# Optimization experiments

Measured on AMD Instinct MI355X. Metric: run time of the kernel, lower is better.

Reference implementation:

```python
import jax, jax.numpy as jnp
import numpy as np

NORM_EPS = 1e-6
QUANT_EPS = 1e-8


def setup_inputs() -> dict:
    key = jax.random.key(0)
    k1, k2 = jax.random.split(key)
    B, S, D_IN, D_OUT = 2, 4096, 2048, 2048
    x = jax.random.normal(k1, (B, S, D_IN), dtype=jnp.float32)
    # master fp32 weights (kaiming-uniform-ish scale)
    weight = jax.random.uniform(k2, (D_OUT, D_IN), dtype=jnp.float32,
                                minval=-1.0, maxval=1.0) * (1.0 / np.sqrt(D_IN))
    norm_weight = jnp.ones((D_IN,), dtype=jnp.float32)
    return {"x": x, "weight": weight, "norm_weight": norm_weight}


def _rmsnorm(x, gain):
    rms = jnp.sqrt(jnp.mean(x * x, axis=-1, keepdims=True) + NORM_EPS)
    return x / rms * gain


def _ternary_quantize(w):
    gamma = jnp.mean(jnp.abs(w))                       # absmean scale (scalar)
    w_q = jnp.clip(jnp.round(w / (gamma + QUANT_EPS)), -1.0, 1.0)
    return w_q, gamma


def reference(x, weight, norm_weight):
    # 1) RMSNorm input
    xn = _rmsnorm(x, norm_weight)
    # 2) ternary-quantize weights {-1,0,+1} with absmean gamma
    w_q, gamma = _ternary_quantize(weight)
    # 3) matmul with ternary weights, 4) scale by gamma
    # xn: [B,S,Din], w_q: [Dout,Din] -> [B,S,Dout]
    return jnp.einsum('bsd,od->bso', xn, w_q) * gamma
```

## Files before the change

### kernel.cpp

```cpp
#include <hip/hip_runtime.h>
#include <hip/hip_bf16.h>
#include <stdint.h>

typedef unsigned short u16;
typedef signed char i8;

#define D_INNER 2048
#define D_OUTER 2048
#define MROWS   8192
#define W_ELEMS (D_OUTER * D_INNER)
#define NPART   1024

#define BM 256
#define BN 256
#define BK 128
#define NKT (D_INNER / BK)
#define SLOT_BYTES 65536
#define LDS_TOTAL  131072

typedef __attribute__((ext_vector_type(4))) float f32x4;
typedef __attribute__((ext_vector_type(4))) int   i32x4;
typedef __attribute__((ext_vector_type(16))) int  i32x16;

__global__ __launch_bounds__(256) void prep_kernel(const float* __restrict__ x,
                            const float* __restrict__ g,
                            const float* __restrict__ w,
                            i8* __restrict__ xn, float* __restrict__ srow,
                            float* __restrict__ partials) {
  int t = threadIdx.x;
  int lane = t & 63, wvi = t >> 6;

  if (blockIdx.x >= MROWS / 4) {
    __shared__ float red[4];
    int p = blockIdx.x - MROWS / 4;
    int base = p * 1024;
    float s = 0.f;
#pragma unroll
    for (int r = 0; r < 4; ++r) {
      f32x4 v = ((const f32x4*)w)[base + r * 256 + t];
      s += fabsf(v[0]) + fabsf(v[1]) + fabsf(v[2]) + fabsf(v[3]);
    }
    for (int off = 32; off; off >>= 1) s += __shfl_down(s, off, 64);
    if (lane == 0) red[wvi] = s;
    __syncthreads();
    if (t == 0) partials[p] = red[0] + red[1] + red[2] + red[3];
    return;
  }

  int row = blockIdx.x * 4 + wvi;
  const f32x4* xr = (const f32x4*)(x + (size_t)row * D_INNER);
  const f32x4* gr = (const f32x4*)g;
  i8* xo = xn + (size_t)row * D_INNER;

  f32x4 v[8], gv[8];
#pragma unroll
  for (int r = 0; r < 8; ++r) {
    v[r]  = __builtin_nontemporal_load(&xr[lane + r * 64]);
    gv[r] = gr[lane + r * 64];
  }
  float s = 0.f, m = 0.f;
#pragma unroll
  for (int r = 0; r < 8; ++r) {
    s += v[r][0]*v[r][0] + v[r][1]*v[r][1] + v[r][2]*v[r][2] + v[r][3]*v[r][3];
    m = fmaxf(m, fmaxf(fmaxf(fabsf(v[r][0]*gv[r][0]), fabsf(v[r][1]*gv[r][1])),
                       fmaxf(fabsf(v[r][2]*gv[r][2]), fabsf(v[r][3]*gv[r][3]))));
  }
#pragma unroll
  for (int off = 32; off; off >>= 1) {
    s += __shfl_xor(s, off, 64);
    m = fmaxf(m, __shfl_xor(m, off, 64));
  }
  float invr = 1.0f / sqrtf(s * (1.0f / (float)D_INNER) + 1e-6f);
  float amax = fmaxf(m * invr, 1e-12f);
  float step = amax * (1.0f / 127.0f);
  float qs   = 127.0f / amax;
  if (lane == 0) srow[row] = step;

#pragma unroll
  for (int r = 0; r < 8; ++r) {
    char4 q;
    float qv;
    qv = fminf(127.f, fmaxf(-127.f, rintf(v[r][0]*invr*gv[r][0]*qs))); q.x = (i8)(int)qv;
    qv = fminf(127.f, fmaxf(-127.f, rintf(v[r][1]*invr*gv[r][1]*qs))); q.y = (i8)(int)qv;
    qv = fminf(127.f, fmaxf(-127.f, rintf(v[r][2]*invr*gv[r][2]*qs))); q.z = (i8)(int)qv;
    qv = fminf(127.f, fmaxf(-127.f, rintf(v[r][3]*invr*gv[r][3]*qs))); q.w = (i8)(int)qv;
    ((char4*)xo)[lane + r * 64] = q;
  }
}

__global__ __launch_bounds__(256) void quant_kernel(const float* __restrict__ w,
                             const float* __restrict__ partials,
                             float* __restrict__ gamma_out, i8* __restrict__ wq) {
  f32x4 pv = ((const f32x4*)partials)[threadIdx.x];
  double d = (double)pv[0] + (double)pv[1] + (double)pv[2] + (double)pv[3];
  for (int off = 32; off; off >>= 1) d += __shfl_down(d, off, 64);
  __shared__ double red[4];
  int lane = threadIdx.x & 63, wvi = threadIdx.x >> 6;
  if (lane == 0) red[wvi] = d;
  __syncthreads();
  double total = red[0] + red[1] + red[2] + red[3];
  float gamma = (float)(total * (1.0 / (double)W_ELEMS));
  float inv = 1.0f / (gamma + 1e-8f);
  if (blockIdx.x == 0 && threadIdx.x == 0) *gamma_out = gamma;

  int tid = blockIdx.x * blockDim.x + threadIdx.x;
  int stride = gridDim.x * blockDim.x;
  for (int i = tid; i < W_ELEMS / 4; i += stride) {
    f32x4 v = ((const f32x4*)w)[i];
    char4 q;
    q.x = (i8)(int)fminf(1.f, fmaxf(-1.f, rintf(v[0] * inv)));
    q.y = (i8)(int)fminf(1.f, fmaxf(-1.f, rintf(v[1] * inv)));
    q.z = (i8)(int)fminf(1.f, fmaxf(-1.f, rintf(v[2] * inv)));
    q.w = (i8)(int)fminf(1.f, fmaxf(-1.f, rintf(v[3] * inv)));
    ((char4*)wq)[i] = q;
  }
}

#define GLDS(SRC, DST) __builtin_amdgcn_global_load_lds( \
    (const __attribute__((address_space(1))) void*)(SRC), \
    (__attribute__((address_space(3))) void*)(DST), 16, 0, 0)
#define WAITVM(N) asm volatile("s_waitcnt vmcnt(" #N ")")
#define BAR()     __builtin_amdgcn_s_barrier()
#define FENCE()   __builtin_amdgcn_sched_barrier(0)

__global__ __launch_bounds__(256, 1) void gemm_bt(const i8* __restrict__ A,
                                                  const i8* __restrict__ Bw,
                                                  const float* __restrict__ gamma_p,
                                                  const float* __restrict__ srow,
                                                  float* __restrict__ C) {
  extern __shared__ i8 lds[];

  int f   = blockIdx.y * 8 + blockIdx.x;
  int xcd = f & 7;
  int gg  = f >> 3;
  int orig = xcd * 32 + gg;
  int nb  = orig & 7;
  int mb  = orig >> 3;
  int bm0 = mb * BM;
  int bn0 = nb * BN;

  int tid  = threadIdx.x;
  int lane = tid & 63;
  int wv   = tid >> 6;
  int wr   = wv >> 1;
  int wc   = wv & 1;
  int l31  = lane & 31;
  int hi   = lane >> 5;

  const i8* Ag = A  + (size_t)bm0 * D_INNER;
  const i8* Bg = Bw + (size_t)bn0 * D_INNER;

  size_t srcx = (size_t)(tid >> 3) * D_INNER + (((tid & 7) ^ ((tid >> 3) & 7)) << 4);

  int rdA = (wr * 128 + l31) * BK;
  int rdB = 32768 + (wc * 128 + l31) * BK;
  int swz[4];
#pragma unroll
  for (int ks = 0; ks < 4; ++ks)
    swz[ks] = (((ks << 1) | hi) ^ (l31 & 7)) << 4;

  i32x16 acc[4][4] = {};
  i32x4 bf_[4][4];

#define GLDS_A(T_, RR, S_) \
    GLDS(Ag + srcx + (size_t)(RR) * (32 * D_INNER) + (size_t)(T_) * BK, \
         lds + (S_) * SLOT_BYTES + (RR) * 4096 + tid * 16)
#define GLDS_B(T_, RR, S_) \
    GLDS(Bg + srcx + (size_t)(RR) * (32 * D_INNER) + (size_t)(T_) * BK, \
         lds + (S_) * SLOT_BYTES + 32768 + (RR) * 4096 + tid * 16)

#define PHASE(T_, P_, DS_) do { \
    if (DS_) { \
      if ((P_) == 0) { GLDS_A(T_+1, 0, (T_+1)&1); GLDS_A(T_+1, 1, (T_+1)&1); \
                       GLDS_A(T_+1, 2, (T_+1)&1); GLDS_B(T_+1, 0, (T_+1)&1); \
                       GLDS_B(T_+1, 1, (T_+1)&1); GLDS_B(T_+1, 2, (T_+1)&1); } \
      if ((P_) == 1) { GLDS_A(T_+1, 3, (T_+1)&1); GLDS_A(T_+1, 4, (T_+1)&1); \
                       GLDS_A(T_+1, 5, (T_+1)&1); GLDS_B(T_+1, 3, (T_+1)&1); \
                       GLDS_B(T_+1, 4, (T_+1)&1); GLDS_B(T_+1, 5, (T_+1)&1); } \
      if ((P_) == 2) { GLDS_A(T_+1, 6, (T_+1)&1); GLDS_A(T_+1, 7, (T_+1)&1); \
                       GLDS_B(T_+1, 6, (T_+1)&1); GLDS_B(T_+1, 7, (T_+1)&1); } \
    } \
    const i8* sl_ = lds + ((T_) & 1) * SLOT_BYTES; \
    if ((P_) == 0) { \
      _Pragma("unroll") for (int ks = 0; ks < 4; ++ks) \
        _Pragma("unroll") for (int nj = 0; nj < 4; ++nj) \
          bf_[ks][nj] = *(const i32x4*)(sl_ + rdB + nj * 4096 + swz[ks]); \
    } \
    i32x4 af_[4]; \
    _Pragma("unroll") for (int ks = 0; ks < 4; ++ks) \
      af_[ks] = *(const i32x4*)(sl_ + rdA + (P_) * 4096 + swz[ks]); \
    __builtin_amdgcn_s_setprio(1); \
    _Pragma("unroll") for (int ks = 0; ks < 4; ++ks) \
      _Pragma("unroll") for (int nj = 0; nj < 4; ++nj) \
        acc[P_][nj] = __builtin_amdgcn_mfma_i32_32x32x32_i8(af_[ks], bf_[ks][nj], acc[P_][nj], 0, 0, 0); \
    __builtin_amdgcn_s_setprio(0); \
  } while (0)

#pragma unroll
  for (int rr = 0; rr < 8; ++rr) { GLDS_A(0, rr, 0); GLDS_B(0, rr, 0); }

  for (int t = 0; t < NKT; ++t) {
    WAITVM(0);
    FENCE();
    BAR();
    FENCE();
    if (t < NKT - 1) {
      PHASE(t, 0, 1); PHASE(t, 1, 1); PHASE(t, 2, 1); PHASE(t, 3, 1);
    } else {
      PHASE(t, 0, 0); PHASE(t, 1, 0); PHASE(t, 2, 0); PHASE(t, 3, 0);
    }
  }

  float gamma = *gamma_p;
#pragma unroll
  for (int mi = 0; mi < 4; ++mi) {
    int rbase = bm0 + wr * 128 + mi * 32 + hi * 4;
    f32x4 sg[4];
#pragma unroll
    for (int q = 0; q < 4; ++q) {
      f32x4 sv = *(const f32x4*)(srow + rbase + q * 8);
      sg[q] = sv * gamma;
    }
#pragma unroll
    for (int nj = 0; nj < 4; ++nj) {
      int colb = bn0 + wc * 128 + nj * 32 + l31;
      i32x16 v = acc[mi][nj];
      float* cp = C + (size_t)rbase * D_OUTER + colb;
#pragma unroll
      for (int q = 0; q < 4; ++q)
#pragma unroll
        for (int rr = 0; rr < 4; ++rr)
          cp[(size_t)(q * 8 + rr) * D_OUTER] = (float)v[q * 4 + rr] * sg[q][rr];
    }
  }
}

extern "C" void kernel_launch(void* const* d_in, const int* in_sizes, int n_in,
                              void* d_out, int out_size, void* d_ws, size_t ws_size,
                              hipStream_t stream) {
  const float* x = (const float*)d_in[0];
  const float* w = (const float*)d_in[1];
  const float* g = (const float*)d_in[2];
  float* out = (float*)d_out;

  float* gamma_p  = (float*)d_ws;
  float* partials = (float*)((char*)d_ws + 64);
  float* srow     = (float*)((char*)d_ws + 8192);
  i8* xn = (i8*)((char*)d_ws + 8192 + 32768);
  i8* wq = (i8*)((char*)d_ws + 8192 + 32768 + (size_t)MROWS * D_INNER);

  static bool attr_set = false;
  if (!attr_set) {
    (void)hipFuncSetAttribute(reinterpret_cast<const void*>(&gemm_bt),
                              hipFuncAttributeMaxDynamicSharedMemorySize, LDS_TOTAL);
    attr_set = true;
  }

  prep_kernel<<<MROWS / 4 + NPART, 256, 0, stream>>>(x, g, w, xn, srow, partials);
  quant_kernel<<<2048, 256, 0, stream>>>(w, partials, gamma_p, wq);
  gemm_bt<<<dim3(8, 32), 256, LDS_TOTAL, stream>>>(xn, wq, gamma_p, srow, out);
}
```

Measured before the change: 161.9 us.

## Restructure int8 GEMM k-loop with double-buffered A fragments and batched prefetch

```diff
diff --git a/kernel.cpp b/kernel.cpp
--- a/kernel.cpp
+++ b/kernel.cpp
@@ -160,7 +160,6 @@
     swz[ks] = (((ks << 1) | hi) ^ (l31 & 7)) << 4;
 
   i32x16 acc[4][4] = {};
-  i32x4 bf_[4][4];
 
 #define GLDS_A(T_, RR, S_) \
     GLDS(Ag + srcx + (size_t)(RR) * (32 * D_INNER) + (size_t)(T_) * BK, \
@@ -169,47 +168,50 @@
     GLDS(Bg + srcx + (size_t)(RR) * (32 * D_INNER) + (size_t)(T_) * BK, \
          lds + (S_) * SLOT_BYTES + 32768 + (RR) * 4096 + tid * 16)
 
-#define PHASE(T_, P_, DS_) do { \
+#define MFMA16(P_, AF) do { \
+    _Pragma("unroll") for (int ks = 0; ks < 4; ++ks) \
+      _Pragma("unroll") for (int nj = 0; nj < 4; ++nj) \
+        acc[P_][nj] = __builtin_amdgcn_mfma_i32_32x32x32_i8( \
+            AF[ks], bf_[ks][nj], acc[P_][nj], 0, 0, 0); \
+  } while (0)
+
+#define TILE(T_, DS_) do { \
+    WAITVM(0);                \
+    FENCE(); \
+    BAR();                    \
+    FENCE(); \
+    const i8* sl_ = lds + ((T_) & 1) * SLOT_BYTES; \
+    i32x4 bf_[4][4]; \
+    _Pragma("unroll") for (int ks = 0; ks < 4; ++ks) \
+      _Pragma("unroll") for (int nj = 0; nj < 4; ++nj) \
+        bf_[ks][nj] = *(const i32x4*)(sl_ + rdB + nj * 4096 + swz[ks]); \
+    i32x4 af0[4], af1[4]; \
+    _Pragma("unroll") for (int ks = 0; ks < 4; ++ks) \
+      af0[ks] = *(const i32x4*)(sl_ + rdA + swz[ks]); \
     if (DS_) { \
-      if ((P_) == 0) { GLDS_A(T_+1, 0, (T_+1)&1); GLDS_A(T_+1, 1, (T_+1)&1); \
-                       GLDS_A(T_+1, 2, (T_+1)&1); GLDS_B(T_+1, 0, (T_+1)&1); \
-                       GLDS_B(T_+1, 1, (T_+1)&1); GLDS_B(T_+1, 2, (T_+1)&1); } \
-      if ((P_) == 1) { GLDS_A(T_+1, 3, (T_+1)&1); GLDS_A(T_+1, 4, (T_+1)&1); \
-                       GLDS_A(T_+1, 5, (T_+1)&1); GLDS_B(T_+1, 3, (T_+1)&1); \
-                       GLDS_B(T_+1, 4, (T_+1)&1); GLDS_B(T_+1, 5, (T_+1)&1); } \
-      if ((P_) == 2) { GLDS_A(T_+1, 6, (T_+1)&1); GLDS_A(T_+1, 7, (T_+1)&1); \
-                       GLDS_B(T_+1, 6, (T_+1)&1); GLDS_B(T_+1, 7, (T_+1)&1); } \
+      _Pragma("unroll") for (int rr = 0; rr < 8; ++rr) { \
+        GLDS_A((T_) + 1, rr, ((T_) + 1) & 1); \
+        GLDS_B((T_) + 1, rr, ((T_) + 1) & 1); \
+      } \
     } \
-    const i8* sl_ = lds + ((T_) & 1) * SLOT_BYTES; \
-    if ((P_) == 0) { \
-      _Pragma("unroll") for (int ks = 0; ks < 4; ++ks) \
-        _Pragma("unroll") for (int nj = 0; nj < 4; ++nj) \
-          bf_[ks][nj] = *(const i32x4*)(sl_ + rdB + nj * 4096 + swz[ks]); \
-    } \
-    i32x4 af_[4]; \
-    _Pragma("unroll") for (int ks = 0; ks < 4; ++ks) \
-      af_[ks] = *(const i32x4*)(sl_ + rdA + (P_) * 4096 + swz[ks]); \
-    __builtin_amdgcn_s_setprio(1); \
-    _Pragma("unroll") for (int ks = 0; ks < 4; ++ks) \
-      _Pragma("unroll") for (int nj = 0; nj < 4; ++nj) \
-        acc[P_][nj] = __builtin_amdgcn_mfma_i32_32x32x32_i8(af_[ks], bf_[ks][nj], acc[P_][nj], 0, 0, 0); \
-    __builtin_amdgcn_s_setprio(0); \
+    _Pragma("unroll") for (int ks = 0; ks < 4; ++ks) \
+      af1[ks] = *(const i32x4*)(sl_ + rdA + 1 * 4096 + swz[ks]); \
+    MFMA16(0, af0); \
+    _Pragma("unroll") for (int ks = 0; ks < 4; ++ks) \
+      af0[ks] = *(const i32x4*)(sl_ + rdA + 2 * 4096 + swz[ks]); \
+    MFMA16(1, af1); \
+    _Pragma("unroll") for (int ks = 0; ks < 4; ++ks) \
+      af1[ks] = *(const i32x4*)(sl_ + rdA + 3 * 4096 + swz[ks]); \
+    MFMA16(2, af0); \
+    MFMA16(3, af1); \
   } while (0)
 
 #pragma unroll
   for (int rr = 0; rr < 8; ++rr) { GLDS_A(0, rr, 0); GLDS_B(0, rr, 0); }
 
-  for (int t = 0; t < NKT; ++t) {
-    WAITVM(0);
-    FENCE();
-    BAR();
-    FENCE();
-    if (t < NKT - 1) {
-      PHASE(t, 0, 1); PHASE(t, 1, 1); PHASE(t, 2, 1); PHASE(t, 3, 1);
-    } else {
-      PHASE(t, 0, 0); PHASE(t, 1, 0); PHASE(t, 2, 0); PHASE(t, 3, 0);
-    }
-  }
+  for (int t = 0; t < NKT - 1; ++t)
+    TILE(t, 1);
+  TILE(NKT - 1, 0);
 
   float gamma = *gamma_p;
 #pragma unroll
```

New measurement: 162.1 us. About the same (+0.1%).

## Shrink GEMM tile to 256x128 with single-buffered LDS for two blocks per CU

Applied to the files above, without the earlier changes.

```diff
diff --git a/kernel.cpp b/kernel.cpp
--- a/kernel.cpp
+++ b/kernel.cpp
@@ -12,11 +12,10 @@
 #define NPART   1024
 
 #define BM 256
-#define BN 256
+#define BN 128
 #define BK 128
 #define NKT (D_INNER / BK)
-#define SLOT_BYTES 65536
-#define LDS_TOTAL  131072
+#define LDS_TOTAL 49152
 
 typedef __attribute__((ext_vector_type(4))) float f32x4;
 typedef __attribute__((ext_vector_type(4))) int   i32x4;
@@ -123,7 +122,7 @@
 #define BAR()     __builtin_amdgcn_s_barrier()
 #define FENCE()   __builtin_amdgcn_sched_barrier(0)
 
-__global__ __launch_bounds__(256, 1) void gemm_bt(const i8* __restrict__ A,
+__global__ __launch_bounds__(256, 2) void gemm_bt(const i8* __restrict__ A,
                                                   const i8* __restrict__ Bw,
                                                   const float* __restrict__ gamma_p,
                                                   const float* __restrict__ srow,
@@ -133,9 +132,9 @@
   int f   = blockIdx.y * 8 + blockIdx.x;
   int xcd = f & 7;
   int gg  = f >> 3;
-  int orig = xcd * 32 + gg;
-  int nb  = orig & 7;
-  int mb  = orig >> 3;
+  int orig = xcd * 64 + gg;
+  int nb  = orig & 15;
+  int mb  = orig >> 4;
   int bm0 = mb * BM;
   int bn0 = nb * BN;
 
@@ -153,61 +152,58 @@
   size_t srcx = (size_t)(tid >> 3) * D_INNER + (((tid & 7) ^ ((tid >> 3) & 7)) << 4);
 
   int rdA = (wr * 128 + l31) * BK;
-  int rdB = 32768 + (wc * 128 + l31) * BK;
+  int rdB = 32768 + (wc * 64 + l31) * BK;
   int swz[4];
 #pragma unroll
   for (int ks = 0; ks < 4; ++ks)
     swz[ks] = (((ks << 1) | hi) ^ (l31 & 7)) << 4;
 
-  i32x16 acc[4][4] = {};
-  i32x4 bf_[4][4];
-
-#define GLDS_A(T_, RR, S_) \
-    GLDS(Ag + srcx + (size_t)(RR) * (32 * D_INNER) + (size_t)(T_) * BK, \
-         lds + (S_) * SLOT_BYTES + (RR) * 4096 + tid * 16)
-#define GLDS_B(T_, RR, S_) \
-    GLDS(Bg + srcx + (size_t)(RR) * (32 * D_INNER) + (size_t)(T_) * BK, \
-         lds + (S_) * SLOT_BYTES + 32768 + (RR) * 4096 + tid * 16)
-
-#define PHASE(T_, P_, DS_) do { \
-    if (DS_) { \
-      if ((P_) == 0) { GLDS_A(T_+1, 0, (T_+1)&1); GLDS_A(T_+1, 1, (T_+1)&1); \
-                       GLDS_A(T_+1, 2, (T_+1)&1); GLDS_B(T_+1, 0, (T_+1)&1); \
-                       GLDS_B(T_+1, 1, (T_+1)&1); GLDS_B(T_+1, 2, (T_+1)&1); } \
-      if ((P_) == 1) { GLDS_A(T_+1, 3, (T_+1)&1); GLDS_A(T_+1, 4, (T_+1)&1); \
-                       GLDS_A(T_+1, 5, (T_+1)&1); GLDS_B(T_+1, 3, (T_+1)&1); \
-                       GLDS_B(T_+1, 4, (T_+1)&1); GLDS_B(T_+1, 5, (T_+1)&1); } \
-      if ((P_) == 2) { GLDS_A(T_+1, 6, (T_+1)&1); GLDS_A(T_+1, 7, (T_+1)&1); \
-                       GLDS_B(T_+1, 6, (T_+1)&1); GLDS_B(T_+1, 7, (T_+1)&1); } \
-    } \
-    const i8* sl_ = lds + ((T_) & 1) * SLOT_BYTES; \
-    if ((P_) == 0) { \
-      _Pragma("unroll") for (int ks = 0; ks < 4; ++ks) \
-        _Pragma("unroll") for (int nj = 0; nj < 4; ++nj) \
-          bf_[ks][nj] = *(const i32x4*)(sl_ + rdB + nj * 4096 + swz[ks]); \
-    } \
-    i32x4 af_[4]; \
-    _Pragma("unroll") for (int ks = 0; ks < 4; ++ks) \
-      af_[ks] = *(const i32x4*)(sl_ + rdA + (P_) * 4096 + swz[ks]); \
+  i32x16 acc[4][2] = {};
+
+#define STAGE(T_) do { \
+    _Pragma("unroll") for (int rr = 0; rr < 8; ++rr) \
+      GLDS(Ag + srcx + (size_t)rr * (32 * D_INNER) + (size_t)(T_) * BK, \
+           lds + rr * 4096 + tid * 16); \
+    _Pragma("unroll") for (int rr = 0; rr < 4; ++rr) \
+      GLDS(Bg + srcx + (size_t)rr * (32 * D_INNER) + (size_t)(T_) * BK, \
+           lds + 32768 + rr * 4096 + tid * 16); \
+  } while (0)
+
+#define MFMA8(P_, AF) do { \
     __builtin_amdgcn_s_setprio(1); \
     _Pragma("unroll") for (int ks = 0; ks < 4; ++ks) \
-      _Pragma("unroll") for (int nj = 0; nj < 4; ++nj) \
-        acc[P_][nj] = __builtin_amdgcn_mfma_i32_32x32x32_i8(af_[ks], bf_[ks][nj], acc[P_][nj], 0, 0, 0); \
+      _Pragma("unroll") for (int nj = 0; nj < 2; ++nj) \
+        acc[P_][nj] = __builtin_amdgcn_mfma_i32_32x32x32_i8( \
+            AF[ks], bf_[ks][nj], acc[P_][nj], 0, 0, 0); \
     __builtin_amdgcn_s_setprio(0); \
   } while (0)
 
-#pragma unroll
-  for (int rr = 0; rr < 8; ++rr) { GLDS_A(0, rr, 0); GLDS_B(0, rr, 0); }
+#define COMPUTE() do { \
+    i32x4 bf_[4][2]; \
+    _Pragma("unroll") for (int ks = 0; ks < 4; ++ks) \
+      _Pragma("unroll") for (int nj = 0; nj < 2; ++nj) \
+        bf_[ks][nj] = *(const i32x4*)(lds + rdB + nj * 4096 + swz[ks]); \
+    _Pragma("unroll") for (int mi = 0; mi < 4; ++mi) { \
+      i32x4 af_[4]; \
+      _Pragma("unroll") for (int ks = 0; ks < 4; ++ks) \
+        af_[ks] = *(const i32x4*)(lds + rdA + mi * 4096 + swz[ks]); \
+      MFMA8(mi, af_); \
+    } \
+  } while (0)
+
+  STAGE(0);
 
   for (int t = 0; t < NKT; ++t) {
     WAITVM(0);
     FENCE();
     BAR();
     FENCE();
+    COMPUTE();
+    FENCE();
     if (t < NKT - 1) {
-      PHASE(t, 0, 1); PHASE(t, 1, 1); PHASE(t, 2, 1); PHASE(t, 3, 1);
-    } else {
-      PHASE(t, 0, 0); PHASE(t, 1, 0); PHASE(t, 2, 0); PHASE(t, 3, 0);
+      BAR();
+      FENCE();
+      STAGE(t + 1);
     }
   }
 
@@ -222,8 +218,8 @@
       sg[q] = sv * gamma;
     }
 #pragma unroll
-    for (int nj = 0; nj < 4; ++nj) {
-      int colb = bn0 + wc * 128 + nj * 32 + l31;
+    for (int nj = 0; nj < 2; ++nj) {
+      int colb = bn0 + wc * 64 + nj * 32 + l31;
       i32x16 v = acc[mi][nj];
       float* cp = C + (size_t)rbase * D_OUTER + colb;
 #pragma unroll
@@ -258,5 +254,5 @@
 
   prep_kernel<<<MROWS / 4 + NPART, 256, 0, stream>>>(x, g, w, xn, srow, partials);
   quant_kernel<<<2048, 256, 0, stream>>>(w, partials, gamma_p, wq);
-  gemm_bt<<<dim3(8, 32), 256, LDS_TOTAL, stream>>>(xn, wq, gamma_p, srow, out);
-}
+  gemm_bt<<<dim3(8, 64), 256, LDS_TOTAL, stream>>>(xn, wq, gamma_p, srow, out);
+}
```

Result: slower. 167.4 us (+3.4%).
